# Kernel tuning notes

Measured on AMD Instinct MI355X. Metric: run time of the kernel, lower is better.

Reference implementation:

```python
import jax, jax.numpy as jnp
import numpy as np

B, N, H, L = 2, 512, 128, 6
NUM_T = 300.0


def setup_inputs() -> dict:
    key = jax.random.key(0)
    ks = iter(jax.random.split(key, 64))
    nrm = lambda *s: jax.random.normal(next(ks), s, dtype=jnp.float32)
    lin = lambda o, i: nrm(o, i) / np.sqrt(i)
    lin3 = lambda o, i: nrm(L, o, i) / np.sqrt(i)  # stacked per-layer weights
    return dict(
        atom_feat=nrm(B, N, 6),
        coord=nrm(B, N, 3),
        radial=jax.random.uniform(next(ks), (B, N, N, 1), dtype=jnp.float32),
        disp=nrm(B, N, N, 3),
        t=jax.random.uniform(next(ks), (B, 1), dtype=jnp.float32) * NUM_T,
        adj_mat=jnp.ones((B, N, N, 1), dtype=bool),
        mask=jnp.ones((B, N), dtype=bool),
        mask2d=jnp.ones((B, N, N, 1), dtype=bool),
        feat_enc_W=lin(H, 6), feat_enc_b=jnp.zeros(H, jnp.float32),
        freq_bands=jnp.linspace(0.0, 1.0, H // 2, dtype=jnp.float32)[None, :],
        combine_W=lin(H, 2 * H), combine_b=jnp.zeros(H, jnp.float32),
        msg_W1=lin3(H, 2 * H + 1), msg_b1=jnp.zeros((L, H), jnp.float32),
        msg_W2=lin3(H, H), msg_b2=jnp.zeros((L, H), jnp.float32),
        feat_W1=lin3(H, 2 * H), feat_b1=jnp.zeros((L, H), jnp.float32),
        feat_W2=lin3(H, H), feat_b2=jnp.zeros((L, H), jnp.float32),
        coord_W1=lin3(H, H), coord_b1=jnp.zeros((L, H), jnp.float32),
        coord_W2=lin3(1, H) * 0.001,  # xavier gain=0.001
        dec_W1=lin(H, H), dec_b1=jnp.zeros(H, jnp.float32),
        dec_W2=lin(3, H), dec_b2=jnp.zeros(3, jnp.float32),
    )


def _forward(atom_feat, coord, radial, disp, t,
             feat_enc_W, feat_enc_b, freq_bands, combine_W, combine_b,
             msg_W1, msg_b1, msg_W2, msg_b2,
             feat_W1, feat_b1, feat_W2, feat_b2,
             coord_W1, coord_b1, coord_W2,
             dec_W1, dec_b1, dec_W2, dec_b2,
             adj_mat, mask, mask2d):
    silu = jax.nn.silu
    radial = 1.0 / (radial + 0.3)  # use_rinv=True
    fenc = atom_feat @ feat_enc_W.T + feat_enc_b            # [B,N,H]
    ang = (t / NUM_T + freq_bands) * (0.5 * jnp.pi)         # [B,H/2]
    tfeat = jnp.concatenate([jnp.sin(ang), jnp.cos(ang)], -1)[:, None, :]
    tfeat = jnp.broadcast_to(tfeat, fenc.shape)
    feat = jnp.concatenate([fenc, tfeat], -1) @ combine_W.T + combine_b
    dt = feat.dtype
    maskf = mask.astype(dt)[..., None]                      # [B,N,1]
    m2f = mask2d.astype(dt)                                 # [B,N,N,1]
    adjf = adj_mat.astype(dt)
    n = feat.shape[1]
    m2nd = m2f * (1.0 - jnp.eye(n, dtype=dt))[None, :, :, None]  # diag removed
    C = jnp.sum(m2nd[:, 0, :, 0], -1, keepdims=True)[:, :, None]  # [B,1,1]

    def step(f, p):
        Wm1, bm1, Wm2, bm2, Wf1, bf1, Wf2, bf2, Wc1, bc1, Wc2 = p
        # fused broadcast-concat -> linear: split Wm1 over [feat_i | feat_j | radial]
        m = silu((f @ Wm1[:, :H].T)[:, :, None, :]
                 + (f @ Wm1[:, H:2 * H].T)[:, None, :, :]
                 + radial * Wm1[:, 2 * H] + bm1)            # [B,N,N,H]
        m = silu(m @ Wm2.T + bm2)
        # coord update (computed per EGCL, discarded by EGNN forward)
        u = silu(m @ Wc1.T + bc1) @ Wc2.T                   # [B,N,N,1]
        cu = C * jnp.sum(jnp.clip(u * disp, -100.0, 100.0) * m2f * m2nd, axis=2)
        msgf = jnp.sum(m * (m2f * adjf), axis=2)            # [B,N,H]
        nf = silu(jnp.concatenate([f, msgf], -1) @ Wf1.T + bf1) @ Wf2.T + bf2
        return nf * maskf, cu * maskf

    feat, _ = jax.lax.scan(step, feat, (msg_W1, msg_b1, msg_W2, msg_b2,
                                        feat_W1, feat_b1, feat_W2, feat_b2,
                                        coord_W1, coord_b1, coord_W2))
    new_feat = (silu(feat @ dec_W1.T + dec_b1) @ dec_W2.T + dec_b2) * maskf
    return new_feat, coord * maskf


def reference(atom_feat, coord, radial, disp, t, adj_mat, mask, mask2d,
              feat_enc_W, feat_enc_b, freq_bands, combine_W, combine_b,
              msg_W1, msg_b1, msg_W2, msg_b2,
              feat_W1, feat_b1, feat_W2, feat_b2,
              coord_W1, coord_b1, coord_W2,
              dec_W1, dec_b1, dec_W2, dec_b2):
    return _forward(atom_feat, coord, radial, disp, t,
                    feat_enc_W, feat_enc_b, freq_bands, combine_W, combine_b,
                    msg_W1, msg_b1, msg_W2, msg_b2,
                    feat_W1, feat_b1, feat_W2, feat_b2,
                    coord_W1, coord_b1, coord_W2,
                    dec_W1, dec_b1, dec_W2, dec_b2,
                    adj_mat, mask, mask2d)
```

## Files before the change

kernel.cpp:

```cpp
#include <hip/hip_runtime.h>
#include <hip/hip_bf16.h>
#include <math.h>


#define BB 2
#define NN 512
#define HH 128
#define LL 6

typedef short bf16x8 __attribute__((ext_vector_type(8)));
typedef float f32x4  __attribute__((ext_vector_type(4)));

__device__ __forceinline__ float silu_f(float x) {
    return x * __builtin_amdgcn_rcpf(1.0f + __expf(-x));
}
__device__ __forceinline__ short f2bf(float x) {
    union { __hip_bfloat16 b; short s; } u; u.b = __float2bfloat16(x); return u.s;
}
__device__ __forceinline__ float lo_bf(unsigned int w) {
    union { unsigned int u; float f; } v; v.u = w << 16; return v.f;
}
__device__ __forceinline__ float hi_bf(unsigned int w) {
    union { unsigned int u; float f; } v; v.u = w & 0xffff0000u; return v.f;
}
__device__ __forceinline__ unsigned int pk2(float a, float b) {
    return ((unsigned int)(unsigned short)f2bf(a)) |
           (((unsigned int)(unsigned short)f2bf(b)) << 16);
}

__global__ __launch_bounds__(128) void k_prep(
    const float* __restrict__ Wm1,  unsigned short* __restrict__ Wm1b,
    float* __restrict__ w3f,
    const float* __restrict__ Wm2,  unsigned short* __restrict__ Wm2b,
    const float* __restrict__ Wf1,  unsigned short* __restrict__ Wf1b,
    const float* __restrict__ Wf2,  unsigned short* __restrict__ Wf2b,
    const float* __restrict__ dW1,  unsigned short* __restrict__ dW1b,
    const float* __restrict__ atom_feat, const float* __restrict__ t,
    const float* __restrict__ feat_enc_W, const float* __restrict__ feat_enc_b,
    const float* __restrict__ freq_bands,
    const float* __restrict__ combine_W, const float* __restrict__ combine_b,
    const float* __restrict__ bm1,
    float* __restrict__ feat, float* __restrict__ Ahat,
    unsigned short* __restrict__ Bvb)
{
    const int blk = blockIdx.x;
    const int h   = threadIdx.x;

    if (blk < 768) {
        const float* srow = Wm1 + (size_t)blk * 257;
        unsigned short* drow = Wm1b + (size_t)blk * 256;
        drow[h]       = (unsigned short)f2bf(srow[h]);
        drow[h + 128] = (unsigned short)f2bf(srow[h + 128]);
        if (h == 0) w3f[blk] = srow[256];
        return;
    }
    if (blk < 3968) {
        const float* src; unsigned short* dst; size_t idx;
        if (blk < 1536)      { src = Wm2; dst = Wm2b; idx = (size_t)(blk - 768)  * 128 + h; }
        else if (blk < 3072) { src = Wf1; dst = Wf1b; idx = (size_t)(blk - 1536) * 128 + h; }
        else if (blk < 3840) { src = Wf2; dst = Wf2b; idx = (size_t)(blk - 3072) * 128 + h; }
        else                 { src = dW1; dst = dW1b; idx = (size_t)(blk - 3840) * 128 + h; }
        dst[idx] = (unsigned short)f2bf(src[idx]);
        return;
    }

    const int row = blk - 3968;
    const int b   = row >> 9;
    __shared__ float cat[2 * HH];
    __shared__ float fr[HH];

    const float* af = atom_feat + row * 6;
    const float* wv = feat_enc_W + h * 6;
    float fe = feat_enc_b[h];
    #pragma unroll
    for (int k = 0; k < 6; ++k) fe = fmaf(af[k], wv[k], fe);
    cat[h] = fe;

    const float tv  = t[b] * (1.0f / 300.0f);
    const float fb  = freq_bands[h & 63];
    const float ang = (tv + fb) * 1.5707963267948966f;
    cat[HH + h] = (h < 64) ? sinf(ang) : cosf(ang);
    __syncthreads();

    const float* cw = combine_W + h * (2 * HH);
    float acc = combine_b[h];
    #pragma unroll 8
    for (int k = 0; k < 2 * HH; ++k) acc = fmaf(cat[k], cw[k], acc);
    feat[row * HH + h] = acc;
    fr[h] = acc;
    __syncthreads();

    const float* wr = Wm1 + h * 257;
    float a = bm1[h], bb = 0.0f;
    #pragma unroll 8
    for (int k = 0; k < HH; ++k) {
        a  = fmaf(fr[k], wr[k], a);
        bb = fmaf(fr[k], wr[HH + k], bb);
    }
    Ahat[row * HH + h] = a;
    Bvb[row * HH + h]  = (unsigned short)f2bf(bb);
}

__global__ __launch_bounds__(256, 2) void k_msg(
    const float* __restrict__ Ahat,
    const unsigned short* __restrict__ Bvb,
    const float* __restrict__ radial,
    const float* __restrict__ w3l,
    const unsigned short* __restrict__ Wm2b,
    const float* __restrict__ bm2,
    float* __restrict__ msgf)
{
    const int tid  = threadIdx.x;
    const int w    = tid >> 6, lane = tid & 63, r = lane & 15, g = lane >> 4;
    const int ip   = w >> 1, kh = w & 1;
    const int i    = blockIdx.x * 2 + ip;
    const int b    = i >> 9;
    const int k0   = kh * 64;
    const int nb   = kh * 4;

    float a_r[2][8], w3r[2][8];
    #pragma unroll
    for (int s = 0; s < 2; ++s) {
        const int kb = k0 + s * 32 + g * 8;
        *(float4*)&a_r[s][0] = *(const float4*)(Ahat + (size_t)i * HH + kb);
        *(float4*)&a_r[s][4] = *(const float4*)(Ahat + (size_t)i * HH + kb + 4);
        *(float4*)&w3r[s][0] = *(const float4*)(w3l + kb);
        *(float4*)&w3r[s][4] = *(const float4*)(w3l + kb + 4);
    }

    bf16x8 bfrag[8][2];
    #pragma unroll
    for (int nrel = 0; nrel < 8; ++nrel) {
        const int na = (nb + nrel) & 7;
        #pragma unroll
        for (int s = 0; s < 2; ++s)
            bfrag[nrel][s] = *(const bf16x8*)(Wm2b + (size_t)(na * 16 + r) * HH
                                              + k0 + s * 32 + g * 8);
    }
    float bm2n[4];
    #pragma unroll
    for (int nl = 0; nl < 4; ++nl) bm2n[nl] = bm2[(nb + nl) * 16 + r];

    const unsigned short* BvB = Bvb + (size_t)b * NN * HH;
    const float* rad = radial + (size_t)i * NN;

    __shared__ __align__(16) float pbuf[2][2][2][4][4][16][4];

    float msgacc[4] = {0.f, 0.f, 0.f, 0.f};

    uint4 bv0 = *(const uint4*)(BvB + (size_t)r * HH + k0 + g * 8);
    uint4 bv1 = *(const uint4*)(BvB + (size_t)r * HH + k0 + 32 + g * 8);
    float radv = rad[r];

    int p = 0;
    for (int c = 0; c < 32; ++c) {
        const float rinv = __builtin_amdgcn_rcpf(radv + 0.3f);
        const uint4 cc0 = bv0, cc1 = bv1;
        if (c < 31) {
            const int j = (c + 1) * 16 + r;
            bv0 = *(const uint4*)(BvB + (size_t)j * HH + k0 + g * 8);
            bv1 = *(const uint4*)(BvB + (size_t)j * HH + k0 + 32 + g * 8);
            radv = rad[j];
        }

        bf16x8 afrag[2];
        #pragma unroll
        for (int s = 0; s < 2; ++s) {
            union { uint4 q; unsigned int dw[4]; } u; u.q = (s ? cc1 : cc0);
            union { bf16x8 v; unsigned int dw[4]; } o;
            #pragma unroll
            for (int d2 = 0; d2 < 4; ++d2) {
                const unsigned int bw = u.dw[d2];
                const float m0 = silu_f(fmaf(rinv, w3r[s][d2 * 2],
                                             a_r[s][d2 * 2]     + lo_bf(bw)));
                const float m1 = silu_f(fmaf(rinv, w3r[s][d2 * 2 + 1],
                                             a_r[s][d2 * 2 + 1] + hi_bf(bw)));
                o.dw[d2] = pk2(m0, m1);
            }
            afrag[s] = o.v;
        }

        #pragma unroll
        for (int nl = 0; nl < 4; ++nl) {
            f32x4 d = {0.f, 0.f, 0.f, 0.f};
            d = __builtin_amdgcn_mfma_f32_16x16x32_bf16(afrag[0], bfrag[4 + nl][0], d, 0, 0, 0);
            d = __builtin_amdgcn_mfma_f32_16x16x32_bf16(afrag[1], bfrag[4 + nl][1], d, 0, 0, 0);
            *(f32x4*)&pbuf[p][ip][kh ^ 1][nl][g][r][0] = d;
        }
        f32x4 dm[4];
        #pragma unroll
        for (int nl = 0; nl < 4; ++nl) {
            f32x4 d = {0.f, 0.f, 0.f, 0.f};
            d = __builtin_amdgcn_mfma_f32_16x16x32_bf16(afrag[0], bfrag[nl][0], d, 0, 0, 0);
            d = __builtin_amdgcn_mfma_f32_16x16x32_bf16(afrag[1], bfrag[nl][1], d, 0, 0, 0);
            dm[nl] = d;
        }
        __syncthreads();
        #pragma unroll
        for (int nl = 0; nl < 4; ++nl) {
            const f32x4 part = *(const f32x4*)&pbuf[p][ip][kh][nl][g][r][0];
            #pragma unroll
            for (int q = 0; q < 4; ++q)
                msgacc[nl] += silu_f(dm[nl][q] + part[q] + bm2n[nl]);
        }
        p ^= 1;
    }

    #pragma unroll
    for (int nl = 0; nl < 4; ++nl) {
        float v = msgacc[nl];
        v += __shfl_xor(v, 16, 64);
        v += __shfl_xor(v, 32, 64);
        msgacc[nl] = v;
    }
    if (lane < 16) {
        #pragma unroll
        for (int nl = 0; nl < 4; ++nl)
            msgf[(size_t)i * HH + (nb + nl) * 16 + lane] = msgacc[nl];
    }
}

__global__ __launch_bounds__(256) void k_row(
    const float* __restrict__ feat,
    const float* __restrict__ msgf,
    const unsigned short* __restrict__ Wf1b, const float* __restrict__ bf1,
    const unsigned short* __restrict__ Wf2b, const float* __restrict__ bf2,
    const unsigned short* __restrict__ Wm1n,
    const float* __restrict__ bm1n,
    float* __restrict__ Ahat, unsigned short* __restrict__ Bvb,
    const unsigned short* __restrict__ dW1b, const float* __restrict__ db1,
    const float* __restrict__ dW2, const float* __restrict__ db2,
    const float* __restrict__ coord, float* __restrict__ out,
    int mode)
{
    const int row0 = blockIdx.x * 16;
    const int tid  = threadIdx.x;
    const int w = tid >> 6, lane = tid & 63, r = lane & 15, g = lane >> 4;
    const int rswz = (r & 7) << 4;

    __shared__ __align__(16) unsigned short catb[16 * 256];
    __shared__ __align__(16) unsigned short hidb[16 * 136];
    __shared__ __align__(16) unsigned short fb[16 * 136];
    __shared__ __align__(16) float decb[16 * 132];

    {
        const int rw = tid >> 4, cs = tid & 15;
        const float* src = (cs < 8) ? (feat + (size_t)(row0 + rw) * HH + cs * 16)
                                    : (msgf + (size_t)(row0 + rw) * HH + (cs - 8) * 16);
        const float4* s4 = (const float4*)src;
        const float4 x0 = s4[0], x1 = s4[1], x2 = s4[2], x3 = s4[3];
        uint4 o0, o1;
        o0.x = pk2(x0.x, x0.y); o0.y = pk2(x0.z, x0.w);
        o0.z = pk2(x1.x, x1.y); o0.w = pk2(x1.z, x1.w);
        o1.x = pk2(x2.x, x2.y); o1.y = pk2(x2.z, x2.w);
        o1.z = pk2(x3.x, x3.y); o1.w = pk2(x3.z, x3.w);
        char* base = (char*)&catb[rw * 256];
        const int sz = (rw & 7) << 4;
        *(uint4*)(base + ((cs * 32)      ^ sz)) = o0;
        *(uint4*)(base + ((cs * 32 + 16) ^ sz)) = o1;
    }
    __syncthreads();

    const int c0 = w * 32 + r, c1 = w * 32 + 16 + r;

    f32x4 d1a = {0,0,0,0}, d1b = {0,0,0,0};
    const char* catp = (const char*)catb;
    #pragma unroll
    for (int s = 0; s < 8; ++s) {
        bf16x8 afr = *(const bf16x8*)(catp + r * 512 + ((s*64 + g*16) ^ rswz));
        d1a = __builtin_amdgcn_mfma_f32_16x16x32_bf16(
                  afr, *(const bf16x8*)(Wf1b + (size_t)c0 * 256 + s*32 + g*8), d1a, 0,0,0);
        d1b = __builtin_amdgcn_mfma_f32_16x16x32_bf16(
                  afr, *(const bf16x8*)(Wf1b + (size_t)c1 * 256 + s*32 + g*8), d1b, 0,0,0);
    }
    {
        const float ba = bf1[c0], bb = bf1[c1];
        #pragma unroll
        for (int q = 0; q < 4; ++q) {
            const int rw = g * 4 + q;
            hidb[rw * 136 + c0] = (unsigned short)f2bf(silu_f(d1a[q] + ba));
            hidb[rw * 136 + c1] = (unsigned short)f2bf(silu_f(d1b[q] + bb));
        }
    }
    __syncthreads();

    f32x4 d2a = {0,0,0,0}, d2b = {0,0,0,0};
    const char* hidp = (const char*)hidb;
    #pragma unroll
    for (int s = 0; s < 4; ++s) {
        bf16x8 afr = *(const bf16x8*)(hidp + r * 272 + s*64 + g*16);
        d2a = __builtin_amdgcn_mfma_f32_16x16x32_bf16(
                  afr, *(const bf16x8*)(Wf2b + (size_t)c0 * 128 + s*32 + g*8), d2a, 0,0,0);
        d2b = __builtin_amdgcn_mfma_f32_16x16x32_bf16(
                  afr, *(const bf16x8*)(Wf2b + (size_t)c1 * 128 + s*32 + g*8), d2b, 0,0,0);
    }
    {
        const float ba = bf2[c0], bb = bf2[c1];
        float* feat_out = (float*)feat;
        #pragma unroll
        for (int q = 0; q < 4; ++q) {
            const int rw = g * 4 + q;
            const float va = d2a[q] + ba, vb = d2b[q] + bb;
            feat_out[(size_t)(row0 + rw) * HH + c0] = va;
            feat_out[(size_t)(row0 + rw) * HH + c1] = vb;
            fb[rw * 136 + c0] = (unsigned short)f2bf(va);
            fb[rw * 136 + c1] = (unsigned short)f2bf(vb);
        }
    }
    __syncthreads();

    const char* fbp = (const char*)fb;
    if (mode == 0) {
        f32x4 daa = {0,0,0,0}, dab = {0,0,0,0}, dba = {0,0,0,0}, dbb = {0,0,0,0};
        #pragma unroll
        for (int s = 0; s < 4; ++s) {
            bf16x8 afr = *(const bf16x8*)(fbp + r * 272 + s*64 + g*16);
            daa = __builtin_amdgcn_mfma_f32_16x16x32_bf16(
                      afr, *(const bf16x8*)(Wm1n + (size_t)c0*256 + s*32 + g*8), daa, 0,0,0);
            dab = __builtin_amdgcn_mfma_f32_16x16x32_bf16(
                      afr, *(const bf16x8*)(Wm1n + (size_t)c1*256 + s*32 + g*8), dab, 0,0,0);
            dba = __builtin_amdgcn_mfma_f32_16x16x32_bf16(
                      afr, *(const bf16x8*)(Wm1n + (size_t)c0*256 + 128 + s*32 + g*8), dba, 0,0,0);
            dbb = __builtin_amdgcn_mfma_f32_16x16x32_bf16(
                      afr, *(const bf16x8*)(Wm1n + (size_t)c1*256 + 128 + s*32 + g*8), dbb, 0,0,0);
        }
        const float ba = bm1n[c0], bb = bm1n[c1];
        #pragma unroll
        for (int q = 0; q < 4; ++q) {
            const int rw = g * 4 + q;
            const size_t i0 = (size_t)(row0 + rw) * HH;
            Ahat[i0 + c0] = daa[q] + ba;
            Ahat[i0 + c1] = dab[q] + bb;
            Bvb[i0 + c0]  = (unsigned short)f2bf(dba[q]);
            Bvb[i0 + c1]  = (unsigned short)f2bf(dbb[q]);
        }
    } else {
        f32x4 dda = {0,0,0,0}, ddb = {0,0,0,0};
        #pragma unroll
        for (int s = 0; s < 4; ++s) {
            bf16x8 afr = *(const bf16x8*)(fbp + r * 272 + s*64 + g*16);
            dda = __builtin_amdgcn_mfma_f32_16x16x32_bf16(
                      afr, *(const bf16x8*)(dW1b + (size_t)c0 * 128 + s*32 + g*8), dda, 0,0,0);
            ddb = __builtin_amdgcn_mfma_f32_16x16x32_bf16(
                      afr, *(const bf16x8*)(dW1b + (size_t)c1 * 128 + s*32 + g*8), ddb, 0,0,0);
        }
        {
            const float ba = db1[c0], bb = db1[c1];
            #pragma unroll
            for (int q = 0; q < 4; ++q) {
                const int rw = g * 4 + q;
                decb[rw * 132 + c0] = silu_f(dda[q] + ba);
                decb[rw * 132 + c1] = silu_f(ddb[q] + bb);
            }
        }
        __syncthreads();
        if (tid < 48) {
            const int rw = tid / 3, c = tid - rw * 3;
            const float4* wr4 = (const float4*)(dW2 + c * HH);
            const float4* h4  = (const float4*)(decb + rw * 132);
            float a0 = db2[c], a1 = 0.f, a2 = 0.f, a3 = 0.f;
            #pragma unroll 8
            for (int k4 = 0; k4 < 32; ++k4) {
                const float4 hv = h4[k4], wv = wr4[k4];
                a0 = fmaf(hv.x, wv.x, a0); a1 = fmaf(hv.y, wv.y, a1);
                a2 = fmaf(hv.z, wv.z, a2); a3 = fmaf(hv.w, wv.w, a3);
            }
            out[(size_t)(row0 + rw) * 3 + c] = (a0 + a1) + (a2 + a3);
        }
        if (tid >= 128 && tid < 176) {
            const int idx = tid - 128;
            const int rw = idx / 3, c = idx - rw * 3;
            out[(size_t)BB * NN * 3 + (size_t)(row0 + rw) * 3 + c] =
                coord[(size_t)(row0 + rw) * 3 + c];
        }
    }
}

extern "C" void kernel_launch(void* const* d_in, const int* in_sizes, int n_in,
                              void* d_out, int out_size, void* d_ws, size_t ws_size,
                              hipStream_t stream) {
    const float* atom_feat  = (const float*)d_in[0];
    const float* coord      = (const float*)d_in[1];
    const float* radial     = (const float*)d_in[2];
    const float* t          = (const float*)d_in[4];
    const float* feat_enc_W = (const float*)d_in[8];
    const float* feat_enc_b = (const float*)d_in[9];
    const float* freq_bands = (const float*)d_in[10];
    const float* combine_W  = (const float*)d_in[11];
    const float* combine_b  = (const float*)d_in[12];
    const float* msg_W1     = (const float*)d_in[13];
    const float* msg_b1     = (const float*)d_in[14];
    const float* msg_W2     = (const float*)d_in[15];
    const float* msg_b2     = (const float*)d_in[16];
    const float* feat_W1    = (const float*)d_in[17];
    const float* feat_b1    = (const float*)d_in[18];
    const float* feat_W2    = (const float*)d_in[19];
    const float* feat_b2    = (const float*)d_in[20];
    const float* dec_W1     = (const float*)d_in[24];
    const float* dec_b1     = (const float*)d_in[25];
    const float* dec_W2     = (const float*)d_in[26];
    const float* dec_b2     = (const float*)d_in[27];

    float* feat = (float*)d_ws;
    float* Ahat = feat + (size_t)BB * NN * HH;
    float* msgf = Ahat + (size_t)BB * NN * HH;
    float* w3f  = msgf + (size_t)BB * NN * HH;
    unsigned short* Bvb  = (unsigned short*)(w3f + LL * HH);
    unsigned short* Wm1b = Bvb  + (size_t)BB * NN * HH;
    unsigned short* Wm2b = Wm1b + (size_t)LL * HH * 256;
    unsigned short* Wf1b = Wm2b + (size_t)LL * HH * HH;
    unsigned short* Wf2b = Wf1b + (size_t)LL * HH * 256;
    unsigned short* dW1b = Wf2b + (size_t)LL * HH * HH;

    k_prep<<<4992, 128, 0, stream>>>(
        msg_W1, Wm1b, w3f, msg_W2, Wm2b, feat_W1, Wf1b, feat_W2, Wf2b,
        dec_W1, dW1b,
        atom_feat, t, feat_enc_W, feat_enc_b, freq_bands, combine_W, combine_b,
        msg_b1, feat, Ahat, Bvb);

    for (int l = 0; l < LL; ++l) {
        k_msg<<<BB * NN / 2, 256, 0, stream>>>(
            Ahat, Bvb, radial, w3f + l * HH,
            Wm2b + (size_t)l * HH * HH, msg_b2 + l * HH, msgf);
        const int last = (l == LL - 1);
        k_row<<<BB * NN / 16, 256, 0, stream>>>(
            feat, msgf,
            Wf1b + (size_t)l * HH * 256, feat_b1 + l * HH,
            Wf2b + (size_t)l * HH * HH,  feat_b2 + l * HH,
            Wm1b + (size_t)(last ? 0 : (l + 1)) * HH * 256,
            msg_b1 + (last ? 0 : (l + 1)) * HH,
            Ahat, Bvb,
            dW1b, dec_b1, dec_W2, dec_b2,
            coord, (float*)d_out,
            last ? 1 : 0);
    }
}
```

Measured before the change: 524.6 us.

## Split prep into vectorized weight pack and MFMA-based feature init kernel

The single prep kernel is split in two. The first packs weights to bf16 with float4 loads and also converts combine_W. The second computes the initial features and the first layer's Ahat/Bvb projections for 16 rows per block using bf16 MFMA instead of per-thread scalar FMA loops over global weights. This adds a kernel launch and replaces the fp32 initial projections with bf16 ones, a small precision loss.

Result: faster. 479.4 us (-8.6%).

```diff
diff --git a/kernel.cpp b/kernel.cpp
--- a/kernel.cpp
+++ b/kernel.cpp
@@ -28,77 +28,151 @@
            (((unsigned int)(unsigned short)f2bf(b)) << 16);
 }
 
-__global__ __launch_bounds__(128) void k_prep(
-    const float* __restrict__ Wm1,  unsigned short* __restrict__ Wm1b,
-    float* __restrict__ w3f,
+__global__ __launch_bounds__(128) void k_pack(
     const float* __restrict__ Wm2,  unsigned short* __restrict__ Wm2b,
     const float* __restrict__ Wf1,  unsigned short* __restrict__ Wf1b,
     const float* __restrict__ Wf2,  unsigned short* __restrict__ Wf2b,
     const float* __restrict__ dW1,  unsigned short* __restrict__ dW1b,
+    const float* __restrict__ cmbW, unsigned short* __restrict__ cmbWb,
+    const float* __restrict__ Wm1,  unsigned short* __restrict__ Wm1b,
+    float* __restrict__ w3f)
+{
+    const int blk = blockIdx.x;
+    const int h   = threadIdx.x;
+
+    if (blk < 864) {
+        const int idx4 = blk * 128 + h;
+        const float* src; unsigned short* dst; int off;
+        if      (idx4 < 24576)  { src = Wm2;  dst = Wm2b;  off = idx4; }
+        else if (idx4 < 73728)  { src = Wf1;  dst = Wf1b;  off = idx4 - 24576; }
+        else if (idx4 < 98304)  { src = Wf2;  dst = Wf2b;  off = idx4 - 73728; }
+        else if (idx4 < 102400) { src = dW1;  dst = dW1b;  off = idx4 - 98304; }
+        else                    { src = cmbW; dst = cmbWb; off = idx4 - 102400; }
+        const float4 v = ((const float4*)src)[off];
+        uint2 o; o.x = pk2(v.x, v.y); o.y = pk2(v.z, v.w);
+        ((uint2*)dst)[off] = o;
+        return;
+    }
+    const int lh = blk - 864;
+    const float* srow = Wm1 + (size_t)lh * 257;
+    unsigned short* drow = Wm1b + (size_t)lh * 256;
+    drow[h]       = (unsigned short)f2bf(srow[h]);
+    drow[h + 128] = (unsigned short)f2bf(srow[h + 128]);
+    if (h == 0) w3f[lh] = srow[256];
+}
+
+__global__ __launch_bounds__(256) void k_init(
     const float* __restrict__ atom_feat, const float* __restrict__ t,
     const float* __restrict__ feat_enc_W, const float* __restrict__ feat_enc_b,
     const float* __restrict__ freq_bands,
-    const float* __restrict__ combine_W, const float* __restrict__ combine_b,
-    const float* __restrict__ bm1,
+    const unsigned short* __restrict__ cmbWb, const float* __restrict__ combine_b,
+    const unsigned short* __restrict__ Wm1b,  const float* __restrict__ bm1,
     float* __restrict__ feat, float* __restrict__ Ahat,
     unsigned short* __restrict__ Bvb)
 {
-    const int blk = blockIdx.x;
-    const int h   = threadIdx.x;
-
-    if (blk < 768) {
-        const float* srow = Wm1 + (size_t)blk * 257;
-        unsigned short* drow = Wm1b + (size_t)blk * 256;
-        drow[h]       = (unsigned short)f2bf(srow[h]);
-        drow[h + 128] = (unsigned short)f2bf(srow[h + 128]);
-        if (h == 0) w3f[blk] = srow[256];
-        return;
-    }
-    if (blk < 3968) {
-        const float* src; unsigned short* dst; size_t idx;
-        if (blk < 1536)      { src = Wm2; dst = Wm2b; idx = (size_t)(blk - 768)  * 128 + h; }
-        else if (blk < 3072) { src = Wf1; dst = Wf1b; idx = (size_t)(blk - 1536) * 128 + h; }
-        else if (blk < 3840) { src = Wf2; dst = Wf2b; idx = (size_t)(blk - 3072) * 128 + h; }
-        else                 { src = dW1; dst = dW1b; idx = (size_t)(blk - 3840) * 128 + h; }
-        dst[idx] = (unsigned short)f2bf(src[idx]);
-        return;
-    }
-
-    const int row = blk - 3968;
-    const int b   = row >> 9;
-    __shared__ float cat[2 * HH];
-    __shared__ float fr[HH];
-
-    const float* af = atom_feat + row * 6;
-    const float* wv = feat_enc_W + h * 6;
-    float fe = feat_enc_b[h];
-    #pragma unroll
-    for (int k = 0; k < 6; ++k) fe = fmaf(af[k], wv[k], fe);
-    cat[h] = fe;
-
-    const float tv  = t[b] * (1.0f / 300.0f);
-    const float fb  = freq_bands[h & 63];
-    const float ang = (tv + fb) * 1.5707963267948966f;
-    cat[HH + h] = (h < 64) ? sinf(ang) : cosf(ang);
+    const int row0 = blockIdx.x * 16;
+    const int b    = row0 >> 9;
+    const int tid  = threadIdx.x;
+    const int w = tid >> 6, lane = tid & 63, r = lane & 15, g = lane >> 4;
+    const int rswz = (r & 7) << 4;
+
+    __shared__ float s_af[96];
+    __shared__ float s_few[768];
+    __shared__ float s_feb[128];
+    __shared__ float s_tf[128];
+    __shared__ __align__(16) unsigned short catb[16 * 256];
+    __shared__ __align__(16) unsigned short fb[16 * 136];
+
+    if (tid < 96) s_af[tid] = atom_feat[row0 * 6 + tid];
+    s_few[tid]       = feat_enc_W[tid];
+    s_few[tid + 256] = feat_enc_W[tid + 256];
+    s_few[tid + 512] = feat_enc_W[tid + 512];
+    if (tid < 128) {
+        s_feb[tid] = feat_enc_b[tid];
+        const float tv  = t[b] * (1.0f / 300.0f);
+        const float ang = (tv + freq_bands[tid & 63]) * 1.5707963267948966f;
+        s_tf[tid] = (tid < 64) ? sinf(ang) : cosf(ang);
+    }
     __syncthreads();
 
-    const float* cw = combine_W + h * (2 * HH);
-    float acc = combine_b[h];
-    #pragma unroll 8
-    for (int k = 0; k < 2 * HH; ++k) acc = fmaf(cat[k], cw[k], acc);
-    feat[row * HH + h] = acc;
-    fr[h] = acc;
+    {
+        const int rw = tid >> 4;
+        const int h0 = (tid & 15) * 8;
+        float f[8];
+        #pragma unroll
+        for (int u = 0; u < 8; ++u) {
+            const int h = h0 + u;
+            float acc = s_feb[h];
+            #pragma unroll
+            for (int k = 0; k < 6; ++k)
+                acc = fmaf(s_af[rw * 6 + k], s_few[h * 6 + k], acc);
+            f[u] = acc;
+        }
+        uint4 o;
+        o.x = pk2(f[0], f[1]); o.y = pk2(f[2], f[3]);
+        o.z = pk2(f[4], f[5]); o.w = pk2(f[6], f[7]);
+        char* base = (char*)&catb[rw * 256];
+        const int sz = (rw & 7) << 4;
+        *(uint4*)(base + ((h0 * 2) ^ sz)) = o;
+        uint4 o2;
+        o2.x = pk2(s_tf[h0],     s_tf[h0 + 1]); o2.y = pk2(s_tf[h0 + 2], s_tf[h0 + 3]);
+        o2.z = pk2(s_tf[h0 + 4], s_tf[h0 + 5]); o2.w = pk2(s_tf[h0 + 6], s_tf[h0 + 7]);
+        *(uint4*)(base + ((256 + h0 * 2) ^ sz)) = o2;
+    }
     __syncthreads();
 
-    const float* wr = Wm1 + h * 257;
-    float a = bm1[h], bb = 0.0f;
-    #pragma unroll 8
-    for (int k = 0; k < HH; ++k) {
-        a  = fmaf(fr[k], wr[k], a);
-        bb = fmaf(fr[k], wr[HH + k], bb);
-    }
-    Ahat[row * HH + h] = a;
-    Bvb[row * HH + h]  = (unsigned short)f2bf(bb);
+    const int c0 = w * 32 + r, c1 = w * 32 + 16 + r;
+
+    f32x4 d1a = {0,0,0,0}, d1b = {0,0,0,0};
+    const char* catp = (const char*)catb;
+    #pragma unroll
+    for (int s = 0; s < 8; ++s) {
+        bf16x8 afr = *(const bf16x8*)(catp + r * 512 + ((s*64 + g*16) ^ rswz));
+        d1a = __builtin_amdgcn_mfma_f32_16x16x32_bf16(
+                  afr, *(const bf16x8*)(cmbWb + (size_t)c0 * 256 + s*32 + g*8), d1a, 0,0,0);
+        d1b = __builtin_amdgcn_mfma_f32_16x16x32_bf16(
+                  afr, *(const bf16x8*)(cmbWb + (size_t)c1 * 256 + s*32 + g*8), d1b, 0,0,0);
+    }
+    {
+        const float ba = combine_b[c0], bb = combine_b[c1];
+        #pragma unroll
+        for (int q = 0; q < 4; ++q) {
+            const int rw = g * 4 + q;
+            const float va = d1a[q] + ba, vb = d1b[q] + bb;
+            feat[(size_t)(row0 + rw) * HH + c0] = va;
+            feat[(size_t)(row0 + rw) * HH + c1] = vb;
+            fb[rw * 136 + c0] = (unsigned short)f2bf(va);
+            fb[rw * 136 + c1] = (unsigned short)f2bf(vb);
+        }
+    }
+    __syncthreads();
+
+    const char* fbp = (const char*)fb;
+    f32x4 daa = {0,0,0,0}, dab = {0,0,0,0}, dba = {0,0,0,0}, dbb = {0,0,0,0};
+    #pragma unroll
+    for (int s = 0; s < 4; ++s) {
+        bf16x8 afr = *(const bf16x8*)(fbp + r * 272 + s*64 + g*16);
+        daa = __builtin_amdgcn_mfma_f32_16x16x32_bf16(
+                  afr, *(const bf16x8*)(Wm1b + (size_t)c0*256 + s*32 + g*8), daa, 0,0,0);
+        dab = __builtin_amdgcn_mfma_f32_16x16x32_bf16(
+                  afr, *(const bf16x8*)(Wm1b + (size_t)c1*256 + s*32 + g*8), dab, 0,0,0);
+        dba = __builtin_amdgcn_mfma_f32_16x16x32_bf16(
+                  afr, *(const bf16x8*)(Wm1b + (size_t)c0*256 + 128 + s*32 + g*8), dba, 0,0,0);
+        dbb = __builtin_amdgcn_mfma_f32_16x16x32_bf16(
+                  afr, *(const bf16x8*)(Wm1b + (size_t)c1*256 + 128 + s*32 + g*8), dbb, 0,0,0);
+    }
+    {
+        const float ba = bm1[c0], bb = bm1[c1];
+        #pragma unroll
+        for (int q = 0; q < 4; ++q) {
+            const int rw = g * 4 + q;
+            const size_t i0 = (size_t)(row0 + rw) * HH;
+            Ahat[i0 + c0] = daa[q] + ba;
+            Ahat[i0 + c1] = dab[q] + bb;
+            Bvb[i0 + c0]  = (unsigned short)f2bf(dba[q]);
+            Bvb[i0 + c1]  = (unsigned short)f2bf(dbb[q]);
+        }
+    }
 }
 
 __global__ __launch_bounds__(256, 2) void k_msg(
@@ -405,18 +479,21 @@
     float* Ahat = feat + (size_t)BB * NN * HH;
     float* msgf = Ahat + (size_t)BB * NN * HH;
     float* w3f  = msgf + (size_t)BB * NN * HH;
-    unsigned short* Bvb  = (unsigned short*)(w3f + LL * HH);
-    unsigned short* Wm1b = Bvb  + (size_t)BB * NN * HH;
-    unsigned short* Wm2b = Wm1b + (size_t)LL * HH * 256;
-    unsigned short* Wf1b = Wm2b + (size_t)LL * HH * HH;
-    unsigned short* Wf2b = Wf1b + (size_t)LL * HH * 256;
-    unsigned short* dW1b = Wf2b + (size_t)LL * HH * HH;
-
-    k_prep<<<4992, 128, 0, stream>>>(
-        msg_W1, Wm1b, w3f, msg_W2, Wm2b, feat_W1, Wf1b, feat_W2, Wf2b,
-        dec_W1, dW1b,
-        atom_feat, t, feat_enc_W, feat_enc_b, freq_bands, combine_W, combine_b,
-        msg_b1, feat, Ahat, Bvb);
+    unsigned short* Bvb   = (unsigned short*)(w3f + LL * HH);
+    unsigned short* Wm1b  = Bvb   + (size_t)BB * NN * HH;
+    unsigned short* Wm2b  = Wm1b  + (size_t)LL * HH * 256;
+    unsigned short* Wf1b  = Wm2b  + (size_t)LL * HH * HH;
+    unsigned short* Wf2b  = Wf1b  + (size_t)LL * HH * 256;
+    unsigned short* dW1b  = Wf2b  + (size_t)LL * HH * HH;
+    unsigned short* cmbWb = dW1b  + (size_t)HH * HH;
+
+    k_pack<<<1632, 128, 0, stream>>>(
+        msg_W2, Wm2b, feat_W1, Wf1b, feat_W2, Wf2b,
+        dec_W1, dW1b, combine_W, cmbWb, msg_W1, Wm1b, w3f);
+
+    k_init<<<BB * NN / 16, 256, 0, stream>>>(
+        atom_feat, t, feat_enc_W, feat_enc_b, freq_bands,
+        cmbWb, combine_b, Wm1b, msg_b1, feat, Ahat, Bvb);
 
     for (int l = 0; l < LL; ++l) {
         k_msg<<<BB * NN / 2, 256, 0, stream>>>(
```
